# Kernel optimization log

Hardware: AMD Instinct MI355X
Metric: run time of the kernel (lower is better)

The kernel has to match this reference:

```python
import jax, jax.numpy as jnp
import numpy as np

N_LEVELS = 16
F = 2                      # n_features_per_level
LOG2_HASHMAP = 19
TABLE_SIZE = 1 << LOG2_HASHMAP
BASE_RES = 16.0
FINEST_RES = 512.0
BOX_MIN, BOX_MAX = -1.0, 1.0
PRIMES = jnp.array([1, 2654435761, 805459861], dtype=jnp.uint32)
# corner offsets, i outer / k inner, matching BOX_OFFSETS_3D ordering
OFFSETS = jnp.array([[i, j, k] for i in (0, 1) for j in (0, 1) for k in (0, 1)], dtype=jnp.int32)  # [8,3]


def _hash(coords):
    # coords: int32 [N,8,3]; torch int32 mul wraps mod 2^32 -> emulate with uint32
    c = coords.astype(jnp.uint32)
    h = (c[..., 0] * PRIMES[0]) ^ (c[..., 1] * PRIMES[1]) ^ (c[..., 2] * PRIMES[2])
    return (h & jnp.uint32(TABLE_SIZE - 1)).astype(jnp.int32)


def setup_inputs() -> dict:
    key = jax.random.key(0)
    k1, k2 = jax.random.split(key)
    x = jax.random.uniform(k1, (1_000_000, 3), dtype=jnp.float32) * 2.0 - 1.0  # inside [-1,1]^3
    # nn.init.uniform_(w, -1e-4, 1e-4)
    tables = (jax.random.uniform(k2, (N_LEVELS, TABLE_SIZE, F), dtype=jnp.float32) * 2.0 - 1.0) * 1e-4
    return {"x": x, "tables": tables}


def reference(x, tables):
    n = x.shape[0]
    b = jnp.exp((jnp.log(FINEST_RES) - jnp.log(BASE_RES)) / (N_LEVELS - 1))
    resolutions = jnp.floor(BASE_RES * b ** jnp.arange(N_LEVELS, dtype=jnp.float32))  # [L]
    xc = jnp.clip(x, BOX_MIN, BOX_MAX)

    def level(res, table):
        grid = (BOX_MAX - BOX_MIN) / res                      # scalar
        bl = jnp.floor((xc - BOX_MIN) / grid).astype(jnp.int32)  # [N,3] bottom-left voxel idx
        vmin = bl.astype(jnp.float32) * grid + BOX_MIN        # [N,3]
        idx = bl[:, None, :] + OFFSETS                        # [N,8,3]
        emb = table[_hash(idx)]                               # [N,8,F] irregular gather
        # weights use original (unclamped) x, as in the torch forward
        w = (x - vmin) / grid                                 # [N,3]
        e = emb.reshape(n, 2, 2, 2, F)
        e = e[:, 0] * (1 - w[:, 0, None, None, None]) + e[:, 1] * w[:, 0, None, None, None]  # [N,2,2,F]
        e = e[:, 0] * (1 - w[:, 1, None, None]) + e[:, 1] * w[:, 1, None, None]              # [N,2,F]
        e = e[:, 0] * (1 - w[:, 2, None]) + e[:, 1] * w[:, 2, None]                          # [N,F]
        return e

    out = jax.vmap(level)(resolutions, tables)  # [L,N,F]
    # torch.cat(x_embedded_all, dim=-1): level-major feature layout
    return jnp.transpose(out, (1, 0, 2)).reshape(n, N_LEVELS * F)
```

## Files before the change

### kernel.cpp

```cpp
#include <hip/hip_runtime.h>
#include <cmath>

#define NL 16
#define NPAIR 7
#define TABLE_SIZE (1u << 19)
#define TABLE_MASK (TABLE_SIZE - 1u)
#define P1 2654435761u
#define P2 805459861u

typedef float f2v __attribute__((ext_vector_type(2)));
typedef float f4v __attribute__((ext_vector_type(4)));
typedef unsigned int u32;
typedef unsigned long long u64;

struct Params {
  float g[NL];
  int R[NPAIR];
  u32 off[NPAIR];
  u32 nE[NPAIR];
  u32 totE;
};

struct Corners { u32 idx[8]; float wx, wy, wz; };

__device__ __forceinline__ Corners make_corners(
    float g, float px, float py, float pz, float qx, float qy, float qz)
{
  Corners c;
  const float fx = floorf((qx + 1.f) / g);
  const float fy = floorf((qy + 1.f) / g);
  const float fz = floorf((qz + 1.f) / g);
  c.wx = (px - (fx * g - 1.f)) / g;
  c.wy = (py - (fy * g - 1.f)) / g;
  c.wz = (pz - (fz * g - 1.f)) / g;
  const u32 hx0 = (u32)(int)fx;
  const u32 hy0 = (u32)(int)fy * P1;
  const u32 hz0 = (u32)(int)fz * P2;
  const u32 hx1 = hx0 + 1u;
  const u32 hy1 = hy0 + P1;
  const u32 hz1 = hz0 + P2;
  c.idx[0] = (hx0 ^ hy0 ^ hz0) & TABLE_MASK;
  c.idx[1] = (hx0 ^ hy0 ^ hz1) & TABLE_MASK;
  c.idx[2] = (hx0 ^ hy1 ^ hz0) & TABLE_MASK;
  c.idx[3] = (hx0 ^ hy1 ^ hz1) & TABLE_MASK;
  c.idx[4] = (hx1 ^ hy0 ^ hz0) & TABLE_MASK;
  c.idx[5] = (hx1 ^ hy0 ^ hz1) & TABLE_MASK;
  c.idx[6] = (hx1 ^ hy1 ^ hz0) & TABLE_MASK;
  c.idx[7] = (hx1 ^ hy1 ^ hz1) & TABLE_MASK;
  return c;
}

__device__ __forceinline__ f2v trilerp8(const f2v e[8], float wx, float wy, float wz) {
  const float ux = 1.f - wx;
  const f2v a00 = e[0] * ux + e[4] * wx;
  const f2v a01 = e[1] * ux + e[5] * wx;
  const f2v a10 = e[2] * ux + e[6] * wx;
  const f2v a11 = e[3] * ux + e[7] * wx;
  const float uy = 1.f - wy;
  const f2v b0 = a00 * uy + a10 * wy;
  const f2v b1 = a01 * uy + a11 * wy;
  const float uz = 1.f - wz;
  return b0 * uz + b1 * wz;
}

__device__ __forceinline__ f2v xpair_eval(
    const f4v* __restrict__ tab4, float g,
    float px, float py, float pz, float qx, float qy, float qz)
{
  const float fx = floorf((qx + 1.f) / g);
  const float fy = floorf((qy + 1.f) / g);
  const float fz = floorf((qz + 1.f) / g);
  const float wx = (px - (fx * g - 1.f)) / g;
  const float wy = (py - (fy * g - 1.f)) / g;
  const float wz = (pz - (fz * g - 1.f)) / g;
  const u32 bx = (u32)(int)fx;
  const u32 y0 = (u32)(int)fy * P1, y1 = y0 + P1;
  const u32 z0 = (u32)(int)fz * P2, z1 = z0 + P2;
  u32 hA[4], hB[4];
  const u32 w00 = y0 ^ z0, w01 = y0 ^ z1, w10 = y1 ^ z0, w11 = y1 ^ z1;
  hA[0] = (bx ^ w00) & TABLE_MASK;  hB[0] = ((bx + 1u) ^ w00) & TABLE_MASK;
  hA[1] = (bx ^ w01) & TABLE_MASK;  hB[1] = ((bx + 1u) ^ w01) & TABLE_MASK;
  hA[2] = (bx ^ w10) & TABLE_MASK;  hB[2] = ((bx + 1u) ^ w10) & TABLE_MASK;
  hA[3] = (bx ^ w11) & TABLE_MASK;  hB[3] = ((bx + 1u) ^ w11) & TABLE_MASK;

  f4v BA[4], BB[4];
#pragma unroll
  for (int c = 0; c < 4; ++c) BA[c] = tab4[hA[c] >> 1];
#pragma unroll
  for (int c = 0; c < 4; ++c) BB[c] = BA[c];
  if (bx & 1u) {
#pragma unroll
    for (int c = 0; c < 4; ++c) BB[c] = tab4[hB[c] >> 1];
  }
  f2v e[8];
#pragma unroll
  for (int c = 0; c < 4; ++c) {
    const bool sA = (hA[c] & 1u) != 0u;
    const bool sB = (hB[c] & 1u) != 0u;
    e[c][0]     = sA ? BA[c][2] : BA[c][0];
    e[c][1]     = sA ? BA[c][3] : BA[c][1];
    e[4 + c][0] = sB ? BB[c][2] : BB[c][0];
    e[4 + c][1] = sB ? BB[c][3] : BB[c][1];
  }
  return trilerp8(e, wx, wy, wz);
}

__device__ __forceinline__ f2v pair_eval(
    const f4v* __restrict__ pt, int R, float g,
    float px, float py, float pz, float qx, float qy, float qz)
{
  const float fx = floorf((qx + 1.f) / g);
  const float fy = floorf((qy + 1.f) / g);
  const float fz = floorf((qz + 1.f) / g);
  const float wx = (px - (fx * g - 1.f)) / g;
  const float wy = (py - (fy * g - 1.f)) / g;
  const float wz = (pz - (fz * g - 1.f)) / g;
  const int bx = (int)fx, by = (int)fy, bz = (int)fz;
  const int s = R + 1;
  const int base = (bx * (R + 2) + by) * s + bz;
  const f4v p00 = pt[base];
  const f4v p01 = pt[base + s];
  const f4v p10 = pt[base + (R + 2) * s];
  const f4v p11 = pt[base + (R + 3) * s];
  const float uz = 1.f - wz;
  const f2v a00 = { p00[0] * uz + p00[2] * wz, p00[1] * uz + p00[3] * wz };
  const f2v a01 = { p01[0] * uz + p01[2] * wz, p01[1] * uz + p01[3] * wz };
  const f2v a10 = { p10[0] * uz + p10[2] * wz, p10[1] * uz + p10[3] * wz };
  const f2v a11 = { p11[0] * uz + p11[2] * wz, p11[1] * uz + p11[3] * wz };
  const float uy = 1.f - wy;
  const f2v b0 = a00 * uy + a01 * wy;
  const f2v b1 = a10 * uy + a11 * wy;
  const float ux = 1.f - wx;
  return b0 * ux + b1 * wx;
}

__global__ __launch_bounds__(256) void rehash_kernel(
    const float* __restrict__ tables, f4v* __restrict__ pt, Params P)
{
  u32 tid = blockIdx.x * 256 + threadIdx.x;
  if (tid >= P.totE) return;
  int l = 0; u32 e = tid;
  while (e >= P.nE[l]) { e -= P.nE[l]; ++l; }
  const u32 R = (u32)P.R[l];
  const u32 vz = e % (R + 1u);
  const u32 t2 = e / (R + 1u);
  const u32 vy = t2 % (R + 2u);
  const u32 vx = t2 / (R + 2u);
  const f2v* tab = (const f2v*)tables + (size_t)l * TABLE_SIZE;
  const u32 h0 = (vx ^ (vy * P1) ^ (vz * P2)) & TABLE_MASK;
  const u32 h1 = (vx ^ (vy * P1) ^ ((vz + 1u) * P2)) & TABLE_MASK;
  const f2v a = tab[h0], b = tab[h1];
  const f4v o = { a[0], a[1], b[0], b[1] };
  pt[P.off[l] + e] = o;
}

__global__ __launch_bounds__(256) void coarse_pass_kernel(
    const float* __restrict__ xin, const f4v* __restrict__ pt,
    f2v* __restrict__ ws, int npts, Params P)
{
  const int n = blockIdx.x * 256 + threadIdx.x;
  if (n >= npts) return;
  const float px = __builtin_nontemporal_load(&xin[3 * n + 0]);
  const float py = __builtin_nontemporal_load(&xin[3 * n + 1]);
  const float pz = __builtin_nontemporal_load(&xin[3 * n + 2]);
  const float qx = fminf(fmaxf(px, -1.f), 1.f);
  const float qy = fminf(fmaxf(py, -1.f), 1.f);
  const float qz = fminf(fmaxf(pz, -1.f), 1.f);
#pragma unroll
  for (int l = 0; l < 5; ++l) {
    const f2v r = pair_eval(pt + P.off[l], P.R[l], P.g[l], px, py, pz, qx, qy, qz);
    __builtin_nontemporal_store(r, ws + (size_t)l * npts + n);
  }
}

__global__ __launch_bounds__(256) void pair_pass_kernel(
    const float* __restrict__ xin, const f4v* __restrict__ pt,
    f2v* __restrict__ wsl, int npts, int strideT, int R, float g)
{
  const int n0 = blockIdx.x * 256 + threadIdx.x;
  const int n1 = n0 + strideT;
  const int c0 = n0 < npts ? n0 : npts - 1;
  const int c1 = n1 < npts ? n1 : npts - 1;
  const float px0 = xin[3 * c0 + 0], py0 = xin[3 * c0 + 1], pz0 = xin[3 * c0 + 2];
  const float px1 = xin[3 * c1 + 0], py1 = xin[3 * c1 + 1], pz1 = xin[3 * c1 + 2];
  const float qx0 = fminf(fmaxf(px0, -1.f), 1.f), qy0 = fminf(fmaxf(py0, -1.f), 1.f), qz0 = fminf(fmaxf(pz0, -1.f), 1.f);
  const float qx1 = fminf(fmaxf(px1, -1.f), 1.f), qy1 = fminf(fmaxf(py1, -1.f), 1.f), qz1 = fminf(fmaxf(pz1, -1.f), 1.f);
  const f2v r0 = pair_eval(pt, R, g, px0, py0, pz0, qx0, qy0, qz0);
  const f2v r1 = pair_eval(pt, R, g, px1, py1, pz1, qx1, qy1, qz1);
  if (n0 < npts) __builtin_nontemporal_store(r0, wsl + n0);
  if (n1 < npts) __builtin_nontemporal_store(r1, wsl + n1);
}

__global__ __launch_bounds__(256) void xpair_pass_kernel(
    const float* __restrict__ xin, const f4v* __restrict__ tab4,
    f2v* __restrict__ wsl, int npts, int strideT, float g)
{
  const int nb = blockIdx.x * 256 + threadIdx.x;
#pragma unroll
  for (int i = 0; i < 4; ++i) {
    const int n = nb + i * strideT;
    const int c = n < npts ? n : npts - 1;
    const float px = xin[3 * c + 0], py = xin[3 * c + 1], pz = xin[3 * c + 2];
    const float qx = fminf(fmaxf(px, -1.f), 1.f);
    const float qy = fminf(fmaxf(py, -1.f), 1.f);
    const float qz = fminf(fmaxf(pz, -1.f), 1.f);
    const f2v r = xpair_eval(tab4, g, px, py, pz, qx, qy, qz);
    if (n < npts) __builtin_nontemporal_store(r, wsl + n);
  }
}

__global__ __launch_bounds__(256) void final_kernel(
    const float* __restrict__ xin, const f4v* __restrict__ tab15,
    const f2v* __restrict__ ws, float* __restrict__ out, int npts, float g15)
{
  __shared__ f2v lds[NL][257];
  const int t = threadIdx.x;
  const int base = blockIdx.x * 256;
  const int n = base + t;
  if (n < npts) {
    const float px = xin[3 * n + 0], py = xin[3 * n + 1], pz = xin[3 * n + 2];
    const float qx = fminf(fmaxf(px, -1.f), 1.f);
    const float qy = fminf(fmaxf(py, -1.f), 1.f);
    const float qz = fminf(fmaxf(pz, -1.f), 1.f);
    const f2v r15 = xpair_eval(tab15, g15, px, py, pz, qx, qy, qz);
#pragma unroll
    for (int l = 0; l < NL - 1; ++l)
      lds[l][t] = __builtin_nontemporal_load(ws + (size_t)l * npts + n);
    lds[NL - 1][t] = r15;
  }
  __syncthreads();
#pragma unroll
  for (int k = 0; k < 8; ++k) {
    const int j4 = t + 256 * k;
    const int p = j4 >> 3;
    const int lp = j4 & 7;
    if (base + p < npts) {
      const f2v a = lds[2 * lp + 0][p];
      const f2v b = lds[2 * lp + 1][p];
      const f4v v = { a[0], a[1], b[0], b[1] };
      __builtin_nontemporal_store(v, (f4v*)(out + (size_t)base * 32) + j4);
    }
  }
}

__global__ __launch_bounds__(256) void hash_embed_fused_kernel(
    const float* __restrict__ xin, const float* __restrict__ tables,
    float* __restrict__ out, int npts, Params P)
{
  int n = blockIdx.x * blockDim.x + threadIdx.x;
  if (n >= npts) return;
  const float px = xin[3 * n + 0], py = xin[3 * n + 1], pz = xin[3 * n + 2];
  const float qx = fminf(fmaxf(px, -1.f), 1.f);
  const float qy = fminf(fmaxf(py, -1.f), 1.f);
  const float qz = fminf(fmaxf(pz, -1.f), 1.f);
  f2v acc[NL];
#pragma unroll
  for (int l = 0; l < NL; ++l) {
    const Corners c = make_corners(P.g[l], px, py, pz, qx, qy, qz);
    const f2v* tab = (const f2v*)tables + (size_t)l * TABLE_SIZE;
    f2v e[8];
#pragma unroll
    for (int j = 0; j < 8; ++j) e[j] = tab[c.idx[j]];
    acc[l] = trilerp8(e, c.wx, c.wy, c.wz);
  }
  f4v* o = (f4v*)(out + (size_t)n * 32);
#pragma unroll
  for (int i = 0; i < 8; ++i) {
    const f4v v = { acc[2 * i][0], acc[2 * i][1], acc[2 * i + 1][0], acc[2 * i + 1][1] };
    o[i] = v;
  }
}

extern "C" void kernel_launch(void* const* d_in, const int* in_sizes, int n_in,
                              void* d_out, int out_size, void* d_ws, size_t ws_size,
                              hipStream_t stream) {
  const float* x = (const float*)d_in[0];
  const float* tables = (const float*)d_in[1];
  float* out = (float*)d_out;
  const int npts = in_sizes[0] / 3;

  Params P;
  {
    const float b = expf((logf(512.0f) - logf(16.0f)) / 15.0f);
    u32 off = 0;
    for (int l = 0; l < NL; ++l) {
      const float r = floorf(16.0f * powf(b, (float)l));
      P.g[l] = 2.0f / r;
      if (l < NPAIR) {
        const int R = (int)r;
        P.R[l] = R;
        P.nE[l] = (u32)((R + 2) * (R + 2) * (R + 1));
        P.off[l] = off;
        off += P.nE[l];
      }
    }
    P.totE = off;
  }

  const size_t ws_needed = (size_t)(NL - 1) * npts * sizeof(f2v);
  const size_t pair_bytes = (size_t)P.totE * sizeof(f4v);
  const size_t out_bytes = (size_t)out_size * sizeof(float);

  if (ws_size >= ws_needed && out_bytes >= pair_bytes) {
    f2v* ws = (f2v*)d_ws;
    f4v* pt = (f4v*)d_out;

    hipLaunchKernelGGL(rehash_kernel, dim3((P.totE + 255) / 256), dim3(256), 0, stream,
                       tables, pt, P);

    const int grid = (npts + 255) / 256;
    hipLaunchKernelGGL(coarse_pass_kernel, dim3(grid), dim3(256), 0, stream,
                       x, pt, ws, npts, P);

    const int grid2 = (npts + 511) / 512;
    const int stride2 = grid2 * 256;
    for (int l = 5; l < NPAIR; ++l)
      hipLaunchKernelGGL(pair_pass_kernel, dim3(grid2), dim3(256), 0, stream,
                         x, pt + P.off[l], ws + (size_t)l * npts, npts, stride2,
                         P.R[l], P.g[l]);

    const int grid4 = (npts + 1023) / 1024;
    const int stride4 = grid4 * 256;
    for (int l = NPAIR; l < NL - 1; ++l)
      hipLaunchKernelGGL(xpair_pass_kernel, dim3(grid4), dim3(256), 0, stream,
                         x, (const f4v*)((const f2v*)tables + (size_t)l * TABLE_SIZE),
                         ws + (size_t)l * npts, npts, stride4, P.g[l]);

    hipLaunchKernelGGL(final_kernel, dim3(grid), dim3(256), 0, stream,
                       x, (const f4v*)((const f2v*)tables + (size_t)15 * TABLE_SIZE),
                       ws, out, npts, P.g[15]);
  } else {
    hipLaunchKernelGGL(hash_embed_fused_kernel, dim3((npts + 255) / 256), dim3(256), 0, stream,
                       x, tables, out, npts, P);
  }
}
```

Baseline: 455.8 us.

## Fuse coarse levels into final kernel and move pair table into workspace

Removes the separate coarse_pass kernel. The five coarse levels are now evaluated inside the final kernel straight from the rehashed pair table, so their results no longer make a round trip through workspace memory. Level 15 moves out of the final kernel into its own xpair pass. The pair table now lives in the workspace instead of the output buffer, which needs a larger workspace and falls back to the fused kernel when the workspace is too small.

New measurement: 441.3 us (median of 2 runs). 3.2% less time.

```diff
diff --git a/kernel.cpp b/kernel.cpp
--- a/kernel.cpp
+++ b/kernel.cpp
@@ -11,7 +11,6 @@
 typedef float f2v __attribute__((ext_vector_type(2)));
 typedef float f4v __attribute__((ext_vector_type(4)));
 typedef unsigned int u32;
-typedef unsigned long long u64;
 
 struct Params {
   float g[NL];
@@ -154,25 +153,6 @@
   pt[P.off[l] + e] = o;
 }
 
-__global__ __launch_bounds__(256) void coarse_pass_kernel(
-    const float* __restrict__ xin, const f4v* __restrict__ pt,
-    f2v* __restrict__ ws, int npts, Params P)
-{
-  const int n = blockIdx.x * 256 + threadIdx.x;
-  if (n >= npts) return;
-  const float px = __builtin_nontemporal_load(&xin[3 * n + 0]);
-  const float py = __builtin_nontemporal_load(&xin[3 * n + 1]);
-  const float pz = __builtin_nontemporal_load(&xin[3 * n + 2]);
-  const float qx = fminf(fmaxf(px, -1.f), 1.f);
-  const float qy = fminf(fmaxf(py, -1.f), 1.f);
-  const float qz = fminf(fmaxf(pz, -1.f), 1.f);
-#pragma unroll
-  for (int l = 0; l < 5; ++l) {
-    const f2v r = pair_eval(pt + P.off[l], P.R[l], P.g[l], px, py, pz, qx, qy, qz);
-    __builtin_nontemporal_store(r, ws + (size_t)l * npts + n);
-  }
-}
-
 __global__ __launch_bounds__(256) void pair_pass_kernel(
     const float* __restrict__ xin, const f4v* __restrict__ pt,
     f2v* __restrict__ wsl, int npts, int strideT, int R, float g)
@@ -210,23 +190,25 @@
 }
 
 __global__ __launch_bounds__(256) void final_kernel(
-    const float* __restrict__ xin, const f4v* __restrict__ tab15,
-    const f2v* __restrict__ ws, float* __restrict__ out, int npts, float g15)
+    const float* __restrict__ xin, const f4v* __restrict__ pt,
+    const f2v* __restrict__ ws, float* __restrict__ out, int npts, Params P)
 {
   __shared__ f2v lds[NL][257];
   const int t = threadIdx.x;
   const int base = blockIdx.x * 256;
   const int n = base + t;
-  if (n < npts) {
-    const float px = xin[3 * n + 0], py = xin[3 * n + 1], pz = xin[3 * n + 2];
+  const int c = n < npts ? n : npts - 1;
+  {
+    const float px = xin[3 * c + 0], py = xin[3 * c + 1], pz = xin[3 * c + 2];
     const float qx = fminf(fmaxf(px, -1.f), 1.f);
     const float qy = fminf(fmaxf(py, -1.f), 1.f);
     const float qz = fminf(fmaxf(pz, -1.f), 1.f);
-    const f2v r15 = xpair_eval(tab15, g15, px, py, pz, qx, qy, qz);
-#pragma unroll
-    for (int l = 0; l < NL - 1; ++l)
-      lds[l][t] = __builtin_nontemporal_load(ws + (size_t)l * npts + n);
-    lds[NL - 1][t] = r15;
+#pragma unroll
+    for (int l = 0; l < 5; ++l)
+      lds[l][t] = pair_eval(pt + P.off[l], P.R[l], P.g[l], px, py, pz, qx, qy, qz);
+#pragma unroll
+    for (int li = 0; li < 11; ++li)
+      lds[5 + li][t] = __builtin_nontemporal_load(ws + (size_t)li * npts + c);
   }
   __syncthreads();
 #pragma unroll
@@ -297,38 +279,34 @@
     P.totE = off;
   }
 
-  const size_t ws_needed = (size_t)(NL - 1) * npts * sizeof(f2v);
-  const size_t pair_bytes = (size_t)P.totE * sizeof(f4v);
-  const size_t out_bytes = (size_t)out_size * sizeof(float);
-
-  if (ws_size >= ws_needed && out_bytes >= pair_bytes) {
+  const size_t slab_bytes = (size_t)11 * npts * sizeof(f2v);
+  const size_t pt_off = (slab_bytes + 255) & ~(size_t)255;
+  const size_t need = pt_off + (size_t)P.totE * sizeof(f4v);
+
+  if (ws_size >= need) {
     f2v* ws = (f2v*)d_ws;
-    f4v* pt = (f4v*)d_out;
+    f4v* pt = (f4v*)((char*)d_ws + pt_off);
 
     hipLaunchKernelGGL(rehash_kernel, dim3((P.totE + 255) / 256), dim3(256), 0, stream,
                        tables, pt, P);
-
-    const int grid = (npts + 255) / 256;
-    hipLaunchKernelGGL(coarse_pass_kernel, dim3(grid), dim3(256), 0, stream,
-                       x, pt, ws, npts, P);
 
     const int grid2 = (npts + 511) / 512;
     const int stride2 = grid2 * 256;
     for (int l = 5; l < NPAIR; ++l)
       hipLaunchKernelGGL(pair_pass_kernel, dim3(grid2), dim3(256), 0, stream,
-                         x, pt + P.off[l], ws + (size_t)l * npts, npts, stride2,
+                         x, pt + P.off[l], ws + (size_t)(l - 5) * npts, npts, stride2,
                          P.R[l], P.g[l]);
 
     const int grid4 = (npts + 1023) / 1024;
     const int stride4 = grid4 * 256;
-    for (int l = NPAIR; l < NL - 1; ++l)
+    for (int l = NPAIR; l < NL; ++l)
       hipLaunchKernelGGL(xpair_pass_kernel, dim3(grid4), dim3(256), 0, stream,
                          x, (const f4v*)((const f2v*)tables + (size_t)l * TABLE_SIZE),
-                         ws + (size_t)l * npts, npts, stride4, P.g[l]);
-
+                         ws + (size_t)(l - 5) * npts, npts, stride4, P.g[l]);
+
+    const int grid = (npts + 255) / 256;
     hipLaunchKernelGGL(final_kernel, dim3(grid), dim3(256), 0, stream,
-                       x, (const f4v*)((const f2v*)tables + (size_t)15 * TABLE_SIZE),
-                       ws, out, npts, P.g[15]);
+                       x, pt, ws, out, npts, P);
   } else {
     hipLaunchKernelGGL(hash_embed_fused_kernel, dim3((npts + 255) / 256), dim3(256), 0, stream,
                        x, tables, out, npts, P);
```
